# Optimization experiments

Measured on AMD Instinct MI355X. Metric: run time of the kernel, lower is better.

The kernel has to match this reference:

```python
import jax, jax.numpy as jnp
import numpy as np

DIM = 256
HEADS = 8
WS = 8            # window size
SHIFT = 4
MLP_HID = 1024
EPS = 1e-5
HEAD_DIM = DIM // HEADS
SCALE = HEAD_DIM ** -0.5
N = WS * WS       # tokens per window


def _rel_pos_index():
    coords = np.stack(np.meshgrid(np.arange(WS), np.arange(WS), indexing='ij'))  # [2,ws,ws]
    flat = coords.reshape(2, -1)                                                  # [2,N]
    rel = flat[:, :, None] - flat[:, None, :]                                     # [2,N,N]
    rel = rel.transpose(1, 2, 0)                                                  # [N,N,2]
    rel[:, :, 0] += WS - 1
    rel[:, :, 1] += WS - 1
    rel[:, :, 0] *= 2 * WS - 1
    return jnp.asarray(rel.sum(-1))                                               # [N,N] int

REL_IDX = _rel_pos_index()


def layernorm(x, g, b):
    mu = x.mean(-1, keepdims=True)
    var = ((x - mu) ** 2).mean(-1, keepdims=True)
    return (x - mu) * jax.lax.rsqrt(var + EPS) * g + b


def setup_inputs() -> dict:
    key = jax.random.key(0)
    ks = jax.random.split(key, 16)
    s = 0.02
    return {
        'x': jax.random.normal(ks[0], (16, 16384, DIM), jnp.float32),
        'qkv_w': jax.random.normal(ks[1], (DIM, 3 * DIM), jnp.float32) * s,
        'qkv_b': jnp.zeros((3 * DIM,), jnp.float32),
        'proj_w': jax.random.normal(ks[2], (DIM, DIM), jnp.float32) * s,
        'proj_b': jnp.zeros((DIM,), jnp.float32),
        'rpb_table': jax.random.normal(ks[3], ((2 * WS - 1) ** 2, HEADS), jnp.float32) * s,
        'ln1_g': jnp.ones((DIM,), jnp.float32),
        'ln1_b': jnp.zeros((DIM,), jnp.float32),
        'ln2_g': jnp.ones((DIM,), jnp.float32),
        'ln2_b': jnp.zeros((DIM,), jnp.float32),
        'mlp_w1': jax.random.normal(ks[4], (DIM, MLP_HID), jnp.float32) * s,
        'mlp_b1': jnp.zeros((MLP_HID,), jnp.float32),
        'mlp_w2': jax.random.normal(ks[5], (MLP_HID, DIM), jnp.float32) * s,
        'mlp_b2': jnp.zeros((DIM,), jnp.float32),
        'H': 128,
        'W': 128,
    }


def reference(x, qkv_w, qkv_b, proj_w, proj_b, rpb_table,
              ln1_g, ln1_b, ln2_g, ln2_b, mlp_w1, mlp_b1, mlp_w2, mlp_b2, H, W):
    B, L, C = x.shape
    shortcut = x

    h = layernorm(x, ln1_g, ln1_b).reshape(B, H, W, C)
    if SHIFT > 0:
        h = jnp.roll(h, (-SHIFT, -SHIFT), axis=(1, 2))

    # window partition: [B,H,W,C] -> [B*nW, N, C]
    h = h.reshape(B, H // WS, WS, W // WS, WS, C).transpose(0, 1, 3, 2, 4, 5)
    xw = h.reshape(-1, N, C)
    Bw = xw.shape[0]

    # window attention
    qkv = (xw @ qkv_w + qkv_b).reshape(Bw, N, 3, HEADS, HEAD_DIM)
    q, k, v = qkv[:, :, 0], qkv[:, :, 1], qkv[:, :, 2]        # [Bw,N,H,D]
    attn = jnp.einsum('bnhd,bmhd->bhnm', q, k) * SCALE         # [Bw,H,N,N]
    bias = rpb_table[REL_IDX.reshape(-1)].reshape(N, N, HEADS).transpose(2, 0, 1)
    attn = jax.nn.softmax(attn + bias[None], axis=-1)
    out = jnp.einsum('bhnm,bmhd->bnhd', attn, v).reshape(Bw, N, C)
    out = out @ proj_w + proj_b

    # window reverse
    out = out.reshape(B, H // WS, W // WS, WS, WS, C).transpose(0, 1, 3, 2, 4, 5).reshape(B, H, W, C)
    if SHIFT > 0:
        out = jnp.roll(out, (SHIFT, SHIFT), axis=(1, 2))
    out = out.reshape(B, L, C)

    h2 = layernorm(out, ln2_g, ln2_b)
    mlp = jax.nn.gelu(h2 @ mlp_w1 + mlp_b1, approximate=False) @ mlp_w2 + mlp_b2
    return shortcut + out + mlp
```

## Files before the change

kernel.cpp:

```cpp
#include <hip/hip_runtime.h>
#include <math.h>

typedef short bfrag __attribute__((ext_vector_type(8)));
typedef float ffrag __attribute__((ext_vector_type(4)));

#define MFMA16(a, b, c) __builtin_amdgcn_mfma_f32_16x16x32_bf16((a), (b), (c), 0, 0, 0)

__device__ __align__(16) unsigned short g_wt[786432];

__device__ __forceinline__ unsigned bf16b(float f) {
  unsigned u = __float_as_uint(f);
  return (u + 0x7FFFu + ((u >> 16) & 1u)) >> 16;
}
__device__ __forceinline__ unsigned pk2(float lo, float hi) {
  return bf16b(lo) | (bf16b(hi) << 16);
}
__device__ __forceinline__ float bf2f(unsigned u) {
  return __uint_as_float(u << 16);
}
__device__ __forceinline__ float gelu_t(float u) {
  const float z = 1.5957691216057308f * (u + 0.044715f * u * u * u);
  return u / (1.f + __expf(-z));
}

__global__ void conv_w(const float* __restrict__ qkv_w, const float* __restrict__ proj_w,
                       const float* __restrict__ w1, const float* __restrict__ w2) {
  const int idx = blockIdx.x * 256 + threadIdx.x;
  const float* src; int c, k2, C, K, ofs;
  if (idx < 98304)       { src = qkv_w;  C = 768;  K = 256;  c = idx % 768;  k2 = idx / 768;  ofs = 0; }
  else if (idx < 131072) { int i = idx - 98304;  src = proj_w; C = 256;  K = 256;  c = i % 256;  k2 = i / 256;  ofs = 196608; }
  else if (idx < 262144) { int i = idx - 131072; src = w1;     C = 1024; K = 256;  c = i % 1024; k2 = i / 1024; ofs = 262144; }
  else                   { int i = idx - 262144; src = w2;     C = 256;  K = 1024; c = i % 256;  k2 = i / 256;  ofs = 524288; }
  const float lo = src[(2 * k2) * C + c];
  const float hi = src[(2 * k2 + 1) * C + c];
  *(unsigned*)&g_wt[ofs + c * K + 2 * k2] = pk2(lo, hi);
}

__device__ __forceinline__ int swz(int row, int col, int C) {
  return row * (C * 2) + ((((col >> 3) ^ (row & 7)) << 4) + ((col & 7) << 1));
}
__device__ __forceinline__ bfrag ldfrag(const char* lds, int outer, int k0, int C) {
  const int l = threadIdx.x & 63;
  return *(const bfrag*)(lds + swz(outer + (l & 15), k0 + ((l >> 4) << 3), C));
}

__device__ __forceinline__ void stage128(char* lds, const unsigned short* __restrict__ src,
                                         long rowBase, int strideShorts, int kOfs) {
  const int wv = threadIdx.x >> 6, l = threadIdx.x & 63;
  #pragma unroll
  for (int p = 0; p < 4; ++p) {
    const int base = wv * 1024 + p * 8192;
    const int off = base + l * 16;
    const int row = off >> 8;
    const int ss = ((off & 255) >> 4) ^ (row & 7);
    const unsigned short* g = src + (rowBase + row) * (long)strideShorts + kOfs + ss * 8;
    __builtin_amdgcn_global_load_lds((const __attribute__((address_space(1))) void*)g,
                                     (__attribute__((address_space(3))) void*)(lds + base),
                                     16, 0, 0);
  }
}

template <int DSTROWB>
__device__ __forceinline__ void glds_stage(char* lds, const unsigned short* src,
                                           int srcRowShorts, int bytes) {
  const int wv = threadIdx.x >> 6, l = threadIdx.x & 63;
  for (int base = wv * 1024; base < bytes; base += 8192) {
    const int off = base + l * 16;
    const int row = off / DSTROWB;
    const int slot = (off % DSTROWB) >> 4;
    const int ss = slot ^ (row & 7);
    const unsigned short* g = src + row * srcRowShorts + ss * 8;
    __builtin_amdgcn_global_load_lds((const __attribute__((address_space(1))) void*)g,
                                     (__attribute__((address_space(3))) void*)(lds + base),
                                     16, 0, 0);
  }
}

__device__ __forceinline__ void mm_core128(const char* AX, const char* BW, ffrag acc[2][4]) {
  const int wv = threadIdx.x >> 6;
  const int rh = wv >> 2, cq = wv & 3;
  #pragma unroll
  for (int ks = 0; ks < 4; ++ks) {
    const bfrag aw0 = ldfrag(BW, cq * 32, ks * 32, 128);
    const bfrag aw1 = ldfrag(BW, cq * 32 + 16, ks * 32, 128);
    #pragma unroll
    for (int nt = 0; nt < 4; ++nt) {
      const bfrag xb = ldfrag(AX, rh * 64 + nt * 16, ks * 32, 128);
      acc[0][nt] = MFMA16(aw0, xb, acc[0][nt]);
      acc[1][nt] = MFMA16(aw1, xb, acc[1][nt]);
    }
  }
}

__device__ __forceinline__ void ln_pack(float d0, float d1, float d2, float d3,
                                        const float* g, const float* bb, int lane,
                                        unsigned& o0, unsigned& o1) {
  float s = d0 + d1 + d2 + d3;
  #pragma unroll
  for (int o = 32; o; o >>= 1) s += __shfl_xor(s, o);
  const float mu = s * (1.f / 256.f);
  d0 -= mu; d1 -= mu; d2 -= mu; d3 -= mu;
  float q = d0 * d0 + d1 * d1 + d2 * d2 + d3 * d3;
  #pragma unroll
  for (int o = 32; o; o >>= 1) q += __shfl_xor(q, o);
  const float vv = q * (1.f / 256.f) + 1e-5f;
  float rs = rsqrtf(vv);
  rs = rs * (1.5f - 0.5f * vv * rs * rs);
  const float4 g4 = *(const float4*)(g + lane * 4);
  const float4 b4 = *(const float4*)(bb + lane * 4);
  o0 = pk2(d0 * rs * g4.x + b4.x, d1 * rs * g4.y + b4.y);
  o1 = pk2(d2 * rs * g4.z + b4.z, d3 * rs * g4.w + b4.w);
}

__global__ __launch_bounds__(512) void ln1_k(const float* __restrict__ x,
    const float* __restrict__ g, const float* __restrict__ bb,
    unsigned short* __restrict__ XB, long rowOfs) {
  const int wv = threadIdx.x >> 6, l = threadIdx.x & 63;
  const long lrow = (long)blockIdx.x * 8 + wv;
  const float4 v = *(const float4*)(x + (rowOfs + lrow) * 256 + l * 4);
  unsigned o0, o1;
  ln_pack(v.x, v.y, v.z, v.w, g, bb, l, o0, o1);
  unsigned short* dp = XB + lrow * 256 + l * 4;
  *(unsigned*)dp = o0; *(unsigned*)(dp + 2) = o1;
}

__global__ __launch_bounds__(512, 4) void gemm_qkv(const unsigned short* __restrict__ XB,
    const float* __restrict__ qkv_b, unsigned short* __restrict__ QKV) {
  __shared__ __align__(16) char smem[65536];
  char* AX = smem; char* BW = smem + 32768;
  const int mb = blockIdx.x, nb = blockIdx.y;
  ffrag acc[2][4];
  #pragma unroll
  for (int a = 0; a < 2; ++a)
    #pragma unroll
    for (int n = 0; n < 4; ++n) { ffrag z = {0.f, 0.f, 0.f, 0.f}; acc[a][n] = z; }
  #pragma unroll
  for (int kc = 0; kc < 2; ++kc) {
    stage128(AX, XB, (long)mb * 128, 256, kc * 128);
    stage128(BW, g_wt, (long)nb * 128, 256, kc * 128);
    __syncthreads();
    mm_core128(AX, BW, acc);
    __syncthreads();
  }
  const int l = threadIdx.x & 63, wv = threadIdx.x >> 6;
  const int rh = wv >> 2, cq = wv & 3;
  const float sc = (nb < 2) ? 0.17677669529663687f : 1.f;
  #pragma unroll
  for (int mt = 0; mt < 2; ++mt) {
    const int cg = nb * 128 + cq * 32 + mt * 16 + ((l >> 4) << 2);
    const float4 bq = *(const float4*)(qkv_b + cg);
    #pragma unroll
    for (int nt = 0; nt < 4; ++nt) {
      const long row = (long)mb * 128 + rh * 64 + nt * 16 + (l & 15);
      unsigned short* dp = QKV + row * 768 + cg;
      *(unsigned*)dp       = pk2((acc[mt][nt][0] + bq.x) * sc, (acc[mt][nt][1] + bq.y) * sc);
      *(unsigned*)(dp + 2) = pk2((acc[mt][nt][2] + bq.z) * sc, (acc[mt][nt][3] + bq.w) * sc);
    }
  }
}

__global__ __launch_bounds__(512, 4) void gemm_proj(const unsigned short* __restrict__ O,
    const float* __restrict__ proj_b, unsigned short* __restrict__ outw) {
  __shared__ __align__(16) char smem[65536];
  char* AX = smem; char* BW = smem + 32768;
  const int mb = blockIdx.x, nb = blockIdx.y;
  ffrag acc[2][4];
  #pragma unroll
  for (int a = 0; a < 2; ++a)
    #pragma unroll
    for (int n = 0; n < 4; ++n) { ffrag z = {0.f, 0.f, 0.f, 0.f}; acc[a][n] = z; }
  #pragma unroll
  for (int kc = 0; kc < 2; ++kc) {
    stage128(AX, O, (long)mb * 128, 256, kc * 128);
    stage128(BW, g_wt + 196608, (long)nb * 128, 256, kc * 128);
    __syncthreads();
    mm_core128(AX, BW, acc);
    __syncthreads();
  }
  const int l = threadIdx.x & 63, wv = threadIdx.x >> 6;
  const int rh = wv >> 2, cq = wv & 3;
  #pragma unroll
  for (int mt = 0; mt < 2; ++mt) {
    const int cg = nb * 128 + cq * 32 + mt * 16 + ((l >> 4) << 2);
    const float4 pb = *(const float4*)(proj_b + cg);
    #pragma unroll
    for (int nt = 0; nt < 4; ++nt) {
      const long row = (long)mb * 128 + rh * 64 + nt * 16 + (l & 15);
      unsigned short* dp = outw + row * 256 + cg;
      *(unsigned*)dp       = pk2(acc[mt][nt][0] + pb.x, acc[mt][nt][1] + pb.y);
      *(unsigned*)(dp + 2) = pk2(acc[mt][nt][2] + pb.z, acc[mt][nt][3] + pb.w);
    }
  }
}

__global__ __launch_bounds__(512, 4) void attn_core(const unsigned short* __restrict__ QKV,
    const float* __restrict__ rpb, unsigned short* __restrict__ O, int bofs) {
  __shared__ __align__(16) char smem[81920];
  char* KL = smem;
  char* VT = smem + 32768;
  char* PB = smem + 65536;
  const int t = threadIdx.x, wv = t >> 6, l = t & 63;
  const int blk = blockIdx.x;
  const int b = blk >> 8, w = blk & 255;
  const int wi = w >> 4, wj = w & 15;
  const int bi0 = wi * 8 + 4, bj0 = wj * 8 + 4;
  const ffrag ZERO4 = {0.f, 0.f, 0.f, 0.f};

  #define SROW(r) (((long)b << 14) + (((bi0 + ((r) >> 3)) & 127) << 7) + ((bj0 + ((r) & 7)) & 127))
  #define GROW(r) (((long)(bofs + b) << 14) + (((bi0 + ((r) >> 3)) & 127) << 7) + ((bj0 + ((r) & 7)) & 127))

  #pragma unroll
  for (int p = 0; p < 4; ++p) {
    const int base = wv * 1024 + p * 8192;
    const int off = base + l * 16;
    const int kv = off >> 9;
    const int ss = ((off & 511) >> 4) ^ (kv & 7);
    const unsigned short* g = QKV + SROW(kv) * 768 + 256 + ss * 8;
    __builtin_amdgcn_global_load_lds((const __attribute__((address_space(1))) void*)g,
                                     (__attribute__((address_space(3))) void*)(KL + base),
                                     16, 0, 0);
  }

  {
    const int rp = t & 31, dh = t >> 5;
    const unsigned short* v0p = QKV + SROW(2 * rp) * 768 + 512 + dh * 16;
    const unsigned short* v1p = QKV + SROW(2 * rp + 1) * 768 + 512 + dh * 16;
    const bfrag a0 = *(const bfrag*)v0p, a1 = *(const bfrag*)(v0p + 8);
    const bfrag c0 = *(const bfrag*)v1p, c1 = *(const bfrag*)(v1p + 8);
    #pragma unroll
    for (int j = 0; j < 8; ++j) {
      const unsigned w0 = ((unsigned)(unsigned short)a0[j]) | (((unsigned)(unsigned short)c0[j]) << 16);
      const unsigned w1 = ((unsigned)(unsigned short)a1[j]) | (((unsigned)(unsigned short)c1[j]) << 16);
      *(unsigned*)(VT + swz(dh * 16 + j, 2 * rp, 64)) = w0;
      *(unsigned*)(VT + swz(dh * 16 + 8 + j, 2 * rp, 64)) = w1;
    }
  }
  __syncthreads();

  const int qt = wv & 3, hh = wv >> 2;
  char* myPB = PB + wv * 2048;
  const int colb = l & 15;
  const int rbase = qt * 16 + ((l >> 4) << 2);

  for (int i = 0; i < 4; ++i) {
    const int h = 2 * i + hh;
    const int hk = h * 32;
    const int qr = qt * 16 + (l & 15);
    const bfrag aq = *(const bfrag*)(QKV + SROW(qr) * 768 + hk + ((l >> 4) << 3));
    ffrag s[4];
    #pragma unroll
    for (int nt = 0; nt < 4; ++nt) {
      const bfrag bk = ldfrag(KL, nt * 16, hk, 256);
      s[nt] = MFMA16(aq, bk, ZERO4);
    }
    float pr[4][4], mx[4], sm[4];
    #pragma unroll
    for (int reg = 0; reg < 4; ++reg) mx[reg] = -3e38f;
    #pragma unroll
    for (int nt = 0; nt < 4; ++nt)
      #pragma unroll
      for (int reg = 0; reg < 4; ++reg) {
        const int rr = rbase + reg, cc = nt * 16 + colb;
        const int idx = ((rr >> 3) - (cc >> 3) + 7) * 15 + ((rr & 7) - (cc & 7) + 7);
        pr[nt][reg] = s[nt][reg] + rpb[idx * 8 + h];
        mx[reg] = fmaxf(mx[reg], pr[nt][reg]);
      }
    #pragma unroll
    for (int reg = 0; reg < 4; ++reg) {
      #pragma unroll
      for (int o = 1; o < 16; o <<= 1) mx[reg] = fmaxf(mx[reg], __shfl_xor(mx[reg], o));
      sm[reg] = 0.f;
    }
    #pragma unroll
    for (int nt = 0; nt < 4; ++nt)
      #pragma unroll
      for (int reg = 0; reg < 4; ++reg) {
        pr[nt][reg] = __expf(pr[nt][reg] - mx[reg]);
        sm[reg] += pr[nt][reg];
      }
    #pragma unroll
    for (int reg = 0; reg < 4; ++reg) {
      #pragma unroll
      for (int o = 1; o < 16; o <<= 1) sm[reg] += __shfl_xor(sm[reg], o);
      sm[reg] = 1.f / sm[reg];
    }
    #pragma unroll
    for (int nt = 0; nt < 4; ++nt)
      #pragma unroll
      for (int reg = 0; reg < 4; ++reg)
        *(unsigned short*)(myPB + swz(((l >> 4) << 2) + reg, nt * 16 + colb, 64)) =
            (unsigned short)bf16b(pr[nt][reg] * sm[reg]);

    ffrag o0 = ZERO4, o1 = ZERO4;
    #pragma unroll
    for (int ks = 0; ks < 2; ++ks) {
      const bfrag ap = ldfrag(myPB, 0, ks * 32, 64);
      const bfrag bv0 = ldfrag(VT, hk, ks * 32, 64);
      const bfrag bv1 = ldfrag(VT, hk + 16, ks * 32, 64);
      o0 = MFMA16(ap, bv0, o0);
      o1 = MFMA16(ap, bv1, o1);
    }
    #pragma unroll
    for (int reg = 0; reg < 4; ++reg) {
      const long orow = GROW(rbase + reg);
      O[orow * 256 + hk + colb] = (unsigned short)bf16b(o0[reg]);
      O[orow * 256 + hk + 16 + colb] = (unsigned short)bf16b(o1[reg]);
    }
  }
  #undef SROW
  #undef GROW
}

__global__ __launch_bounds__(512, 4) void swin_mlp(
    const float* __restrict__ x, const unsigned short* __restrict__ outw,
    const float* __restrict__ ln2g, const float* __restrict__ ln2b,
    const float* __restrict__ b1, const float* __restrict__ b2,
    float* __restrict__ y)
{
  __shared__ __align__(16) char smem[73728];
  char* H2 = smem;
  char* WS = smem + 32768;
  char* HD = smem + 65536;
  const int t = threadIdx.x, wv = t >> 6, l = t & 63;
  const long base = (long)blockIdx.x << 6;

  #pragma unroll
  for (int i = 0; i < 8; ++i) {
    const int r = wv * 8 + i;
    const uint2 raw = *(const uint2*)(outw + (base + r) * 256 + l * 4);
    unsigned o0, o1;
    ln_pack(bf2f(raw.x & 0xFFFFu), bf2f(raw.x >> 16), bf2f(raw.y & 0xFFFFu), bf2f(raw.y >> 16),
            ln2g, ln2b, l, o0, o1);
    *(unsigned*)(H2 + swz(r, l * 4, 256)) = o0;
    *(unsigned*)(H2 + swz(r, l * 4 + 2, 256)) = o1;
  }
  __syncthreads();

  const int mq = wv >> 1, nq = (wv & 1) << 1;

  ffrag acc2[2][4];
  #pragma unroll
  for (int mt = 0; mt < 2; ++mt)
    #pragma unroll
    for (int nt = 0; nt < 4; ++nt) { ffrag z = {0.f, 0.f, 0.f, 0.f}; acc2[mt][nt] = z; }

  for (int ch = 0; ch < 16; ++ch) {
    glds_stage<512>(WS, g_wt + 262144 + ch * 64 * 256, 256, 32768);
    __syncthreads();
    ffrag a1[2];
    { ffrag z = {0.f, 0.f, 0.f, 0.f}; a1[0] = z; a1[1] = z; }
    #pragma unroll
    for (int ks = 0; ks < 8; ++ks) {
      const bfrag a = ldfrag(WS, mq * 16, ks * 32, 256);
      const bfrag bb0 = ldfrag(H2, nq * 16, ks * 32, 256);
      const bfrag bb1 = ldfrag(H2, (nq + 1) * 16, ks * 32, 256);
      a1[0] = MFMA16(a, bb0, a1[0]);
      a1[1] = MFMA16(a, bb1, a1[1]);
    }
    __syncthreads();

    glds_stage<128>(WS, g_wt + 524288 + ch * 64, 1024, 32768);
    const int c0 = mq * 16 + ((l >> 4) << 2);
    const float4 b14 = *(const float4*)(b1 + ch * 64 + c0);
    #pragma unroll
    for (int nt = 0; nt < 2; ++nt) {
      const int rr = (nq + nt) * 16 + (l & 15);
      const float g0 = gelu_t(a1[nt][0] + b14.x);
      const float g1 = gelu_t(a1[nt][1] + b14.y);
      const float g2 = gelu_t(a1[nt][2] + b14.z);
      const float g3 = gelu_t(a1[nt][3] + b14.w);
      *(unsigned*)(HD + swz(rr, c0, 64)) = pk2(g0, g1);
      *(unsigned*)(HD + swz(rr, c0 + 2, 64)) = pk2(g2, g3);
    }
    __syncthreads();

    #pragma unroll
    for (int ks = 0; ks < 2; ++ks) {
      const bfrag am0 = ldfrag(WS, (wv * 2) * 16, ks * 32, 64);
      const bfrag am1 = ldfrag(WS, (wv * 2 + 1) * 16, ks * 32, 64);
      #pragma unroll
      for (int nt = 0; nt < 4; ++nt) {
        const bfrag bb = ldfrag(HD, nt * 16, ks * 32, 64);
        acc2[0][nt] = MFMA16(am0, bb, acc2[0][nt]);
        acc2[1][nt] = MFMA16(am1, bb, acc2[1][nt]);
      }
    }
    __syncthreads();
  }

  #pragma unroll
  for (int mt = 0; mt < 2; ++mt) {
    const int c0 = (wv * 2 + mt) * 16 + ((l >> 4) << 2);
    const float4 b24 = *(const float4*)(b2 + c0);
    #pragma unroll
    for (int nt = 0; nt < 4; ++nt) {
      const long row = base + nt * 16 + (l & 15);
      const float4 xv = *(const float4*)(x + row * 256 + c0);
      const uint2 ov = *(const uint2*)(outw + row * 256 + c0);
      float4 res;
      res.x = acc2[mt][nt][0] + b24.x + xv.x + bf2f(ov.x & 0xFFFFu);
      res.y = acc2[mt][nt][1] + b24.y + xv.y + bf2f(ov.x >> 16);
      res.z = acc2[mt][nt][2] + b24.z + xv.z + bf2f(ov.y & 0xFFFFu);
      res.w = acc2[mt][nt][3] + b24.w + xv.w + bf2f(ov.y >> 16);
      *(float4*)(y + row * 256 + c0) = res;
    }
  }
}

extern "C" void kernel_launch(void* const* d_in, const int* in_sizes, int n_in,
                              void* d_out, int out_size, void* d_ws, size_t ws_size,
                              hipStream_t stream) {
  (void)in_sizes; (void)n_in; (void)out_size; (void)ws_size;
  const float* x      = (const float*)d_in[0];
  const float* qkv_w  = (const float*)d_in[1];
  const float* qkv_b  = (const float*)d_in[2];
  const float* proj_w = (const float*)d_in[3];
  const float* proj_b = (const float*)d_in[4];
  const float* rpb    = (const float*)d_in[5];
  const float* ln1g   = (const float*)d_in[6];
  const float* ln1b   = (const float*)d_in[7];
  const float* ln2g   = (const float*)d_in[8];
  const float* ln2b   = (const float*)d_in[9];
  const float* w1     = (const float*)d_in[10];
  const float* b1     = (const float*)d_in[11];
  const float* w2     = (const float*)d_in[12];
  const float* b2     = (const float*)d_in[13];
  float* y = (float*)d_out;
  char* ws = (char*)d_ws;

  unsigned short* XB   = (unsigned short*)(ws);
  unsigned short* QKV  = (unsigned short*)(ws + 33554432);
  unsigned short* Obuf = (unsigned short*)(ws + 134217728);
  unsigned short* outw = (unsigned short*)(ws);

  hipLaunchKernelGGL(conv_w, dim3(1536), dim3(256), 0, stream, qkv_w, proj_w, w1, w2);
  for (int g = 0; g < 4; ++g) {
    hipLaunchKernelGGL(ln1_k, dim3(8192), dim3(512), 0, stream,
                       x, ln1g, ln1b, XB, (long)g * 65536);
    hipLaunchKernelGGL(gemm_qkv, dim3(512, 6), dim3(512), 0, stream, XB, qkv_b, QKV);
    hipLaunchKernelGGL(attn_core, dim3(1024), dim3(512), 0, stream, QKV, rpb, Obuf, g * 4);
  }
  hipLaunchKernelGGL(gemm_proj, dim3(2048, 2), dim3(512), 0, stream, Obuf, proj_b, outw);
  hipLaunchKernelGGL(swin_mlp, dim3(4096), dim3(512), 0, stream,
                     x, outw, ln2g, ln2b, b1, b2, y);
}
```

Baseline: 1.238 ms.

## Load MLP weight fragments directly from global memory and double-buffer hidden tile

The MLP kernel no longer stages W1 and W2 chunks into LDS. Each lane now reads its MFMA weight fragments straight from global memory, where the weights should stay cache-resident. The hidden GELU tile alternates between two LDS buffers, which drops three of the four block barriers per chunk and cuts LDS from 72KB to 48KB, allowing more resident blocks. In exchange, global loads sit on the MFMA critical path and weight reads are duplicated across waves, relying on the caches to absorb them.

```diff
diff --git a/kernel.cpp b/kernel.cpp
--- a/kernel.cpp
+++ b/kernel.cpp
@@ -54,22 +54,6 @@
     const int row = off >> 8;
     const int ss = ((off & 255) >> 4) ^ (row & 7);
     const unsigned short* g = src + (rowBase + row) * (long)strideShorts + kOfs + ss * 8;
-    __builtin_amdgcn_global_load_lds((const __attribute__((address_space(1))) void*)g,
-                                     (__attribute__((address_space(3))) void*)(lds + base),
-                                     16, 0, 0);
-  }
-}
-
-template <int DSTROWB>
-__device__ __forceinline__ void glds_stage(char* lds, const unsigned short* src,
-                                           int srcRowShorts, int bytes) {
-  const int wv = threadIdx.x >> 6, l = threadIdx.x & 63;
-  for (int base = wv * 1024; base < bytes; base += 8192) {
-    const int off = base + l * 16;
-    const int row = off / DSTROWB;
-    const int slot = (off % DSTROWB) >> 4;
-    const int ss = slot ^ (row & 7);
-    const unsigned short* g = src + row * srcRowShorts + ss * 8;
     __builtin_amdgcn_global_load_lds((const __attribute__((address_space(1))) void*)g,
                                      (__attribute__((address_space(3))) void*)(lds + base),
                                      16, 0, 0);
@@ -317,10 +301,10 @@
     const float* __restrict__ b1, const float* __restrict__ b2,
     float* __restrict__ y)
 {
-  __shared__ __align__(16) char smem[73728];
+  __shared__ __align__(16) char smem[49152];
   char* H2 = smem;
-  char* WS = smem + 32768;
-  char* HD = smem + 65536;
+  char* HD0 = smem + 32768;
+  char* HD1 = smem + 40960;
   const int t = threadIdx.x, wv = t >> 6, l = t & 63;
   const long base = (long)blockIdx.x << 6;
 
@@ -337,6 +321,9 @@
   __syncthreads();
 
   const int mq = wv >> 1, nq = (wv & 1) << 1;
+  const int kHi = (l >> 4) << 3;
+  const int aRow = mq * 16 + (l & 15);
+  const int m0 = wv * 32 + (l & 15);
 
   ffrag acc2[2][4];
   #pragma unroll
@@ -345,21 +332,19 @@
     for (int nt = 0; nt < 4; ++nt) { ffrag z = {0.f, 0.f, 0.f, 0.f}; acc2[mt][nt] = z; }
 
   for (int ch = 0; ch < 16; ++ch) {
-    glds_stage<512>(WS, g_wt + 262144 + ch * 64 * 256, 256, 32768);
-    __syncthreads();
+    const unsigned short* w1p = g_wt + 262144 + (long)(ch * 64 + aRow) * 256 + kHi;
     ffrag a1[2];
     { ffrag z = {0.f, 0.f, 0.f, 0.f}; a1[0] = z; a1[1] = z; }
     #pragma unroll
     for (int ks = 0; ks < 8; ++ks) {
-      const bfrag a = ldfrag(WS, mq * 16, ks * 32, 256);
+      const bfrag a = *(const bfrag*)(w1p + ks * 32);
       const bfrag bb0 = ldfrag(H2, nq * 16, ks * 32, 256);
       const bfrag bb1 = ldfrag(H2, (nq + 1) * 16, ks * 32, 256);
       a1[0] = MFMA16(a, bb0, a1[0]);
       a1[1] = MFMA16(a, bb1, a1[1]);
     }
-    __syncthreads();
-
-    glds_stage<128>(WS, g_wt + 524288 + ch * 64, 1024, 32768);
+
+    char* hd = (ch & 1) ? HD1 : HD0;
     const int c0 = mq * 16 + ((l >> 4) << 2);
     const float4 b14 = *(const float4*)(b1 + ch * 64 + c0);
     #pragma unroll
@@ -369,23 +354,23 @@
       const float g1 = gelu_t(a1[nt][1] + b14.y);
       const float g2 = gelu_t(a1[nt][2] + b14.z);
       const float g3 = gelu_t(a1[nt][3] + b14.w);
-      *(unsigned*)(HD + swz(rr, c0, 64)) = pk2(g0, g1);
-      *(unsigned*)(HD + swz(rr, c0 + 2, 64)) = pk2(g2, g3);
+      *(unsigned*)(hd + swz(rr, c0, 64)) = pk2(g0, g1);
+      *(unsigned*)(hd + swz(rr, c0 + 2, 64)) = pk2(g2, g3);
     }
     __syncthreads();
 
+    const unsigned short* w2p = g_wt + 524288 + (long)m0 * 1024 + ch * 64 + kHi;
     #pragma unroll
     for (int ks = 0; ks < 2; ++ks) {
-      const bfrag am0 = ldfrag(WS, (wv * 2) * 16, ks * 32, 64);
-      const bfrag am1 = ldfrag(WS, (wv * 2 + 1) * 16, ks * 32, 64);
+      const bfrag am0 = *(const bfrag*)(w2p + ks * 32);
+      const bfrag am1 = *(const bfrag*)(w2p + 16 * 1024 + ks * 32);
       #pragma unroll
       for (int nt = 0; nt < 4; ++nt) {
-        const bfrag bb = ldfrag(HD, nt * 16, ks * 32, 64);
+        const bfrag bb = ldfrag(hd, nt * 16, ks * 32, 64);
         acc2[0][nt] = MFMA16(am0, bb, acc2[0][nt]);
         acc2[1][nt] = MFMA16(am1, bb, acc2[1][nt]);
       }
     }
-    __syncthreads();
   }
 
   #pragma unroll
```

Result: slower. 1.465 ms (+18.3%).

## Fuse output projection GEMM into the MLP kernel

Applied to the files above, without the earlier changes.

Drops the separate gemm_proj kernel. The swin_mlp kernel now computes the projection of attention outputs for its 64-row tile itself, keeps the fp32 result in registers for the residual add, and stages a bf16 copy in LDS to feed LayerNorm 2. This removes the HBM round trip of the bf16 projection output and one kernel launch. In exchange each MLP block also loads proj weights and does extra MFMA work, and the residual now uses the unrounded fp32 projection. The W2 chunk staging is also moved after the GELU writes so it overlaps them.

```diff
diff --git a/kernel.cpp b/kernel.cpp
--- a/kernel.cpp
+++ b/kernel.cpp
@@ -159,40 +159,6 @@
   }
 }
 
-__global__ __launch_bounds__(512, 4) void gemm_proj(const unsigned short* __restrict__ O,
-    const float* __restrict__ proj_b, unsigned short* __restrict__ outw) {
-  __shared__ __align__(16) char smem[65536];
-  char* AX = smem; char* BW = smem + 32768;
-  const int mb = blockIdx.x, nb = blockIdx.y;
-  ffrag acc[2][4];
-  #pragma unroll
-  for (int a = 0; a < 2; ++a)
-    #pragma unroll
-    for (int n = 0; n < 4; ++n) { ffrag z = {0.f, 0.f, 0.f, 0.f}; acc[a][n] = z; }
-  #pragma unroll
-  for (int kc = 0; kc < 2; ++kc) {
-    stage128(AX, O, (long)mb * 128, 256, kc * 128);
-    stage128(BW, g_wt + 196608, (long)nb * 128, 256, kc * 128);
-    __syncthreads();
-    mm_core128(AX, BW, acc);
-    __syncthreads();
-  }
-  const int l = threadIdx.x & 63, wv = threadIdx.x >> 6;
-  const int rh = wv >> 2, cq = wv & 3;
-  #pragma unroll
-  for (int mt = 0; mt < 2; ++mt) {
-    const int cg = nb * 128 + cq * 32 + mt * 16 + ((l >> 4) << 2);
-    const float4 pb = *(const float4*)(proj_b + cg);
-    #pragma unroll
-    for (int nt = 0; nt < 4; ++nt) {
-      const long row = (long)mb * 128 + rh * 64 + nt * 16 + (l & 15);
-      unsigned short* dp = outw + row * 256 + cg;
-      *(unsigned*)dp       = pk2(acc[mt][nt][0] + pb.x, acc[mt][nt][1] + pb.y);
-      *(unsigned*)(dp + 2) = pk2(acc[mt][nt][2] + pb.z, acc[mt][nt][3] + pb.w);
-    }
-  }
-}
-
 __global__ __launch_bounds__(512, 4) void attn_core(const unsigned short* __restrict__ QKV,
     const float* __restrict__ rpb, unsigned short* __restrict__ O, int bofs) {
   __shared__ __align__(16) char smem[81920];
@@ -312,32 +278,72 @@
 }
 
 __global__ __launch_bounds__(512, 4) void swin_mlp(
-    const float* __restrict__ x, const unsigned short* __restrict__ outw,
+    const float* __restrict__ x, const unsigned short* __restrict__ O,
     const float* __restrict__ ln2g, const float* __restrict__ ln2b,
+    const float* __restrict__ proj_b,
     const float* __restrict__ b1, const float* __restrict__ b2,
     float* __restrict__ y)
 {
   __shared__ __align__(16) char smem[73728];
-  char* H2 = smem;
-  char* WS = smem + 32768;
-  char* HD = smem + 65536;
+  char* R1 = smem;
+  char* R2 = smem + 32768;
+  char* R3 = smem + 65536;
   const int t = threadIdx.x, wv = t >> 6, l = t & 63;
   const long base = (long)blockIdx.x << 6;
 
+  ffrag po[2][4];
+  #pragma unroll
+  for (int mt = 0; mt < 2; ++mt)
+    #pragma unroll
+    for (int nt = 0; nt < 4; ++nt) { ffrag z = {0.f, 0.f, 0.f, 0.f}; po[mt][nt] = z; }
+
+  for (int kc = 0; kc < 4; ++kc) {
+    glds_stage<128>(R1, g_wt + 196608 + kc * 64, 256, 32768);
+    glds_stage<128>(R3, O + base * 256 + kc * 64, 256, 8192);
+    __syncthreads();
+    #pragma unroll
+    for (int ks = 0; ks < 2; ++ks) {
+      const bfrag am0 = ldfrag(R1, (wv * 2) * 16, ks * 32, 64);
+      const bfrag am1 = ldfrag(R1, (wv * 2 + 1) * 16, ks * 32, 64);
+      #pragma unroll
+      for (int nt = 0; nt < 4; ++nt) {
+        const bfrag bb = ldfrag(R3, nt * 16, ks * 32, 64);
+        po[0][nt] = MFMA16(am0, bb, po[0][nt]);
+        po[1][nt] = MFMA16(am1, bb, po[1][nt]);
+      }
+    }
+    __syncthreads();
+  }
+
+  #pragma unroll
+  for (int mt = 0; mt < 2; ++mt) {
+    const int c0 = (wv * 2 + mt) * 16 + ((l >> 4) << 2);
+    const float4 pb4 = *(const float4*)(proj_b + c0);
+    #pragma unroll
+    for (int nt = 0; nt < 4; ++nt) {
+      po[mt][nt][0] += pb4.x; po[mt][nt][1] += pb4.y;
+      po[mt][nt][2] += pb4.z; po[mt][nt][3] += pb4.w;
+      const int rr = nt * 16 + (l & 15);
+      *(unsigned*)(R2 + swz(rr, c0, 256)) = pk2(po[mt][nt][0], po[mt][nt][1]);
+      *(unsigned*)(R2 + swz(rr, c0 + 2, 256)) = pk2(po[mt][nt][2], po[mt][nt][3]);
+    }
+  }
+  __syncthreads();
+
   #pragma unroll
   for (int i = 0; i < 8; ++i) {
     const int r = wv * 8 + i;
-    const uint2 raw = *(const uint2*)(outw + (base + r) * 256 + l * 4);
+    const unsigned raw0 = *(const unsigned*)(R2 + swz(r, l * 4, 256));
+    const unsigned raw1 = *(const unsigned*)(R2 + swz(r, l * 4 + 2, 256));
     unsigned o0, o1;
-    ln_pack(bf2f(raw.x & 0xFFFFu), bf2f(raw.x >> 16), bf2f(raw.y & 0xFFFFu), bf2f(raw.y >> 16),
+    ln_pack(bf2f(raw0 & 0xFFFFu), bf2f(raw0 >> 16), bf2f(raw1 & 0xFFFFu), bf2f(raw1 >> 16),
             ln2g, ln2b, l, o0, o1);
-    *(unsigned*)(H2 + swz(r, l * 4, 256)) = o0;
-    *(unsigned*)(H2 + swz(r, l * 4 + 2, 256)) = o1;
+    *(unsigned*)(R1 + swz(r, l * 4, 256)) = o0;
+    *(unsigned*)(R1 + swz(r, l * 4 + 2, 256)) = o1;
   }
   __syncthreads();
 
   const int mq = wv >> 1, nq = (wv & 1) << 1;
-
   ffrag acc2[2][4];
   #pragma unroll
   for (int mt = 0; mt < 2; ++mt)
@@ -345,21 +351,20 @@
     for (int nt = 0; nt < 4; ++nt) { ffrag z = {0.f, 0.f, 0.f, 0.f}; acc2[mt][nt] = z; }
 
   for (int ch = 0; ch < 16; ++ch) {
-    glds_stage<512>(WS, g_wt + 262144 + ch * 64 * 256, 256, 32768);
+    glds_stage<512>(R2, g_wt + 262144 + ch * 64 * 256, 256, 32768);
     __syncthreads();
     ffrag a1[2];
     { ffrag z = {0.f, 0.f, 0.f, 0.f}; a1[0] = z; a1[1] = z; }
     #pragma unroll
     for (int ks = 0; ks < 8; ++ks) {
-      const bfrag a = ldfrag(WS, mq * 16, ks * 32, 256);
-      const bfrag bb0 = ldfrag(H2, nq * 16, ks * 32, 256);
-      const bfrag bb1 = ldfrag(H2, (nq + 1) * 16, ks * 32, 256);
+      const bfrag a = ldfrag(R2, mq * 16, ks * 32, 256);
+      const bfrag bb0 = ldfrag(R1, nq * 16, ks * 32, 256);
+      const bfrag bb1 = ldfrag(R1, (nq + 1) * 16, ks * 32, 256);
       a1[0] = MFMA16(a, bb0, a1[0]);
       a1[1] = MFMA16(a, bb1, a1[1]);
     }
     __syncthreads();
 
-    glds_stage<128>(WS, g_wt + 524288 + ch * 64, 1024, 32768);
     const int c0 = mq * 16 + ((l >> 4) << 2);
     const float4 b14 = *(const float4*)(b1 + ch * 64 + c0);
     #pragma unroll
@@ -369,18 +374,19 @@
       const float g1 = gelu_t(a1[nt][1] + b14.y);
       const float g2 = gelu_t(a1[nt][2] + b14.z);
       const float g3 = gelu_t(a1[nt][3] + b14.w);
-      *(unsigned*)(HD + swz(rr, c0, 64)) = pk2(g0, g1);
-      *(unsigned*)(HD + swz(rr, c0 + 2, 64)) = pk2(g2, g3);
-    }
+      *(unsigned*)(R3 + swz(rr, c0, 64)) = pk2(g0, g1);
+      *(unsigned*)(R3 + swz(rr, c0 + 2, 64)) = pk2(g2, g3);
+    }
+    glds_stage<128>(R2, g_wt + 524288 + ch * 64, 1024, 32768);
     __syncthreads();
 
     #pragma unroll
     for (int ks = 0; ks < 2; ++ks) {
-      const bfrag am0 = ldfrag(WS, (wv * 2) * 16, ks * 32, 64);
-      const bfrag am1 = ldfrag(WS, (wv * 2 + 1) * 16, ks * 32, 64);
+      const bfrag am0 = ldfrag(R2, (wv * 2) * 16, ks * 32, 64);
+      const bfrag am1 = ldfrag(R2, (wv * 2 + 1) * 16, ks * 32, 64);
       #pragma unroll
       for (int nt = 0; nt < 4; ++nt) {
-        const bfrag bb = ldfrag(HD, nt * 16, ks * 32, 64);
+        const bfrag bb = ldfrag(R3, nt * 16, ks * 32, 64);
         acc2[0][nt] = MFMA16(am0, bb, acc2[0][nt]);
         acc2[1][nt] = MFMA16(am1, bb, acc2[1][nt]);
       }
@@ -396,12 +402,11 @@
     for (int nt = 0; nt < 4; ++nt) {
       const long row = base + nt * 16 + (l & 15);
       const float4 xv = *(const float4*)(x + row * 256 + c0);
-      const uint2 ov = *(const uint2*)(outw + row * 256 + c0);
       float4 res;
-      res.x = acc2[mt][nt][0] + b24.x + xv.x + bf2f(ov.x & 0xFFFFu);
-      res.y = acc2[mt][nt][1] + b24.y + xv.y + bf2f(ov.x >> 16);
-      res.z = acc2[mt][nt][2] + b24.z + xv.z + bf2f(ov.y & 0xFFFFu);
-      res.w = acc2[mt][nt][3] + b24.w + xv.w + bf2f(ov.y >> 16);
+      res.x = acc2[mt][nt][0] + b24.x + xv.x + po[mt][nt][0];
+      res.y = acc2[mt][nt][1] + b24.y + xv.y + po[mt][nt][1];
+      res.z = acc2[mt][nt][2] + b24.z + xv.z + po[mt][nt][2];
+      res.w = acc2[mt][nt][3] + b24.w + xv.w + po[mt][nt][3];
       *(float4*)(y + row * 256 + c0) = res;
     }
   }
@@ -431,7 +436,6 @@
   unsigned short* XB   = (unsigned short*)(ws);
   unsigned short* QKV  = (unsigned short*)(ws + 33554432);
   unsigned short* Obuf = (unsigned short*)(ws + 134217728);
-  unsigned short* outw = (unsigned short*)(ws);
 
   hipLaunchKernelGGL(conv_w, dim3(1536), dim3(256), 0, stream, qkv_w, proj_w, w1, w2);
   for (int g = 0; g < 4; ++g) {
@@ -440,7 +444,6 @@
     hipLaunchKernelGGL(gemm_qkv, dim3(512, 6), dim3(512), 0, stream, XB, qkv_b, QKV);
     hipLaunchKernelGGL(attn_core, dim3(1024), dim3(512), 0, stream, QKV, rpb, Obuf, g * 4);
   }
-  hipLaunchKernelGGL(gemm_proj, dim3(2048, 2), dim3(512), 0, stream, Obuf, proj_b, outw);
   hipLaunchKernelGGL(swin_mlp, dim3(4096), dim3(512), 0, stream,
-                     x, outw, ln2g, ln2b, b1, b2, y);
-}
+                     x, Obuf, ln2g, ln2b, proj_b, b1, b2, y);
+}
```

Result: faster. 1.206 ms (-2.6%).
